# Kernel optimization log

Measured on AMD Instinct MI355X. Metric: run time of the kernel, lower is better.

The kernel has to match this reference:

```python
import jax, jax.numpy as jnp
import numpy as np


def _top_k_mask(matrix, k):
    # top-k along last dim, then scatter 1s into a zero mask (faithful to torch scatter_)
    D = matrix.shape[-1]
    flat = matrix.reshape(-1, D)                       # [N, D]
    _, idx = jax.lax.top_k(flat, k)                    # [N, k]
    rows = jnp.arange(flat.shape[0])[:, None]          # [N, 1]
    mask = jnp.zeros_like(flat).at[rows, idx].set(1.0)  # scatter ones
    return (flat * mask).reshape(matrix.shape)


def setup_inputs() -> dict:
    key = jax.random.key(0)
    x = jax.random.normal(key, (4, 4096, 4096), dtype=jnp.float32)
    return {"x": x, "k": 512}


def reference(x, k):
    g = jax.nn.gelu(x, approximate=False)  # torch F.gelu default is exact (erf) gelu
    return _top_k_mask(g, k)
```

## Files before the change

### kernel.cpp

```cpp
#include <hip/hip_runtime.h>

#define TG_D    4096
#define TG_BLK  256
#define TG_CAP  896
#define TG_T0   0.90f
#define TG_P16G 0xBF40u

__device__ __forceinline__ unsigned tg_key(float f) {
  unsigned b = __float_as_uint(f);
  return (b & 0x80000000u) ? ~b : (b | 0x80000000u);
}
__device__ __forceinline__ unsigned tg_dec(unsigned k) {
  return (k & 0x80000000u) ? (k & 0x7FFFFFFFu) : ~k;
}

__device__ __forceinline__ float tg_gelu(float x) {
#pragma clang fp contract(off)
  float d  = x / 0x1.6a09e6p+0f;
  float xc = fmaxf(fminf(d, 4.0f), -4.0f);
  float x2 = xc * xc;
  float p = -2.72614225801306e-10f;
  p = __builtin_fmaf(p, x2,  2.77068142495902e-08f);
  p = __builtin_fmaf(p, x2, -2.10102402082508e-06f);
  p = __builtin_fmaf(p, x2, -5.69250639462346e-05f);
  p = __builtin_fmaf(p, x2, -7.34990630326855e-04f);
  p = __builtin_fmaf(p, x2, -2.95459980854025e-03f);
  p = __builtin_fmaf(p, x2, -1.60960333262415e-02f);
  float q = -1.45660718464996e-05f;
  q = __builtin_fmaf(q, x2, -2.13374055278905e-04f);
  q = __builtin_fmaf(q, x2, -1.68282697438203e-03f);
  q = __builtin_fmaf(q, x2, -7.37332916720468e-03f);
  q = __builtin_fmaf(q, x2, -1.42647390514189e-02f);
  float num = xc * p;
  float e   = num / q;
  float s   = e + 1.0f;
  float m   = x * s;
  return m * 0.5f;
}

__device__ __forceinline__ void tg_pick_byte(unsigned (*h)[256], unsigned* wtot,
                                             unsigned* sel, unsigned kRem,
                                             int tid, int lane, int wv) {
  __syncthreads();
  unsigned cb = h[0][tid] + h[1][tid] + h[2][tid] + h[3][tid];
  unsigned v = cb;
#pragma unroll
  for (int d = 1; d < 64; d <<= 1) {
    unsigned o = __shfl_down(v, d, 64);
    v += (lane + d < 64) ? o : 0u;
  }
  if (lane == 0) wtot[wv] = v;
  __syncthreads();
  unsigned hi = 0;
#pragma unroll
  for (int w = 0; w < 4; ++w)
    if (w > wv) hi += wtot[w];
  unsigned sGE = v + hi, sGT = sGE - cb;
  if (sGE >= kRem && sGT < kRem) { sel[0] = (unsigned)tid; sel[1] = sGT; sel[2] = cb; }
  __syncthreads();
}

__global__ __launch_bounds__(TG_BLK) void topk_gelu_kernel(
    const float* __restrict__ x, const int* __restrict__ kptr,
    float* __restrict__ out) {
  __shared__ unsigned       ckey[TG_CAP];
  __shared__ unsigned short cidx[TG_CAP];
  __shared__ alignas(16) unsigned char uraw[TG_D * 4];
  __shared__ unsigned       skey[64];
  __shared__ unsigned short scidx[64];
  __shared__ unsigned short scpos[64];
  __shared__ unsigned       tieMask[128];
  __shared__ unsigned       wtot[4];
  __shared__ unsigned       sel[3];
  __shared__ unsigned       cnt2, mCnt;

  float*    cx  = (float*)uraw;
  unsigned (*hist)[256] = (unsigned (*)[256])(uraw + sizeof(float) * TG_CAP);
  float*    obuf = (float*)uraw;

  const int tid = threadIdx.x, lane = tid & 63, wv = tid >> 6;
  const unsigned k = (unsigned)(*kptr);
  const float* xr   = x   + (size_t)blockIdx.x * TG_D;
  float*       outr = out + (size_t)blockIdx.x * TG_D;

  hist[0][tid] = 0; hist[1][tid] = 0; hist[2][tid] = 0; hist[3][tid] = 0;
  if (tid == 0) { cnt2 = 0; mCnt = 0; sel[0] = 0; sel[1] = 0; sel[2] = 0; }

  float xv[16];
#pragma unroll
  for (int c = 0; c < 4; ++c) {
    float4 v = reinterpret_cast<const float4*>(xr)[tid + c * TG_BLK];
    xv[4*c+0] = v.x; xv[4*c+1] = v.y; xv[4*c+2] = v.z; xv[4*c+3] = v.w;
  }

  unsigned candMask = 0;
#pragma unroll
  for (int e = 0; e < 16; ++e)
    if (xv[e] >= TG_T0) candMask |= (1u << e);
  const unsigned cnt = (unsigned)__popc(candMask);
  unsigned inc = cnt;
#pragma unroll
  for (int d = 1; d < 64; d <<= 1) {
    unsigned o = __shfl_up(inc, d, 64);
    if (lane >= d) inc += o;
  }
  if (lane == 63) wtot[wv] = inc;
  __syncthreads();
  unsigned base = inc - cnt;
#pragma unroll
  for (int w = 0; w < 4; ++w) if (w < wv) base += wtot[w];
  const unsigned n0 = wtot[0] + wtot[1] + wtot[2] + wtot[3];
  const unsigned nC = n0 < (unsigned)TG_CAP ? n0 : (unsigned)TG_CAP;

  if (n0 <= (unsigned)TG_CAP) {
    unsigned p = base;
#pragma unroll
    for (int e = 0; e < 16; ++e)
      if (candMask & (1u << e)) {
        cx[p]   = xv[e];
        cidx[p] = (unsigned short)((tid + (e >> 2) * TG_BLK) * 4 + (e & 3));
        ++p;
      }
  }
  __syncthreads();

  unsigned myc2 = 0;
  for (unsigned i = tid; i < nC; i += TG_BLK) {
    unsigned kk = tg_key(tg_gelu(cx[i]));
    ckey[i] = kk;
    if (kk >= 0xC0000000u) ++myc2;
    else atomicAdd(&hist[wv][(kk >> 16) & 255], 1u);
  }
#pragma unroll
  for (int d = 1; d < 64; d <<= 1) {
    unsigned o = __shfl_down(myc2, d, 64);
    myc2 += (lane + d < 64) ? o : 0u;
  }
  if (lane == 0 && myc2) atomicAdd(&cnt2, myc2);
  __syncthreads();

  const unsigned c2v  = cnt2;
  const unsigned kRem = k - c2v;
  unsigned cb = hist[0][tid] + hist[1][tid] + hist[2][tid] + hist[3][tid];
  unsigned v = cb;
#pragma unroll
  for (int d = 1; d < 64; d <<= 1) {
    unsigned o = __shfl_down(v, d, 64);
    v += (lane + d < 64) ? o : 0u;
  }
  if (lane == 0) wtot[wv] = v;
  __syncthreads();
  unsigned hi = 0;
#pragma unroll
  for (int w = 0; w < 4; ++w) if (w > wv) hi += wtot[w];
  {
    unsigned sGE = v + hi, sGT = sGE - cb;
    if (sGE >= kRem && sGT < kRem) { sel[0] = (unsigned)tid; sel[1] = sGT; sel[2] = cb; }
  }
  __syncthreads();

  const unsigned p16   = 0xBF00u | sel[0];
  const unsigned kRem2 = kRem - sel[1];
  const unsigned m     = sel[2];
  const bool slow = (n0 > (unsigned)TG_CAP) || (c2v >= k) || (p16 < TG_P16G) ||
                    (m > 64u) || (kRem2 == 0u) || (kRem2 > m);

  if (slow) {
    unsigned gk[16];
#pragma unroll
    for (int e = 0; e < 16; ++e) gk[e] = tg_key(tg_gelu(xv[e]));
    unsigned prefix = 0, kRemS = k;
#pragma unroll
    for (int ps = 0; ps < 4; ++ps) {
      const int shift = 24 - 8 * ps;
      __syncthreads();
      hist[0][tid] = 0; hist[1][tid] = 0; hist[2][tid] = 0; hist[3][tid] = 0;
      __syncthreads();
      const unsigned pmask = ps ? (0xFFFFFFFFu << (shift + 8)) : 0u;
#pragma unroll
      for (int e = 0; e < 16; ++e)
        if ((gk[e] & pmask) == prefix) atomicAdd(&hist[wv][(gk[e] >> shift) & 255], 1u);
      tg_pick_byte(hist, wtot, sel, kRemS, tid, lane, wv);
      prefix |= sel[0] << shift;
      kRemS  -= sel[1];
    }
    const unsigned Tg = prefix, kRemF = kRemS, cntEq = sel[2];
    const bool needTie = (cntEq != kRemF);
    if (needTie) {
      if (tid < 128) tieMask[tid] = 0;
      __syncthreads();
#pragma unroll
      for (int e = 0; e < 16; ++e)
        if (gk[e] == Tg) {
          unsigned s = (unsigned)((tid + (e >> 2) * TG_BLK) * 4 + (e & 3));
          atomicOr(&tieMask[s >> 5], 1u << (s & 31));
        }
      __syncthreads();
    }
#pragma unroll
    for (int c = 0; c < 4; ++c) {
      float r[4];
#pragma unroll
      for (int j = 0; j < 4; ++j) {
        const int e = 4 * c + j;
        unsigned kk = gk[e];
        bool keep = kk > Tg;
        if (!keep && kk == Tg) {
          if (!needTie) keep = true;
          else {
            unsigned s = (unsigned)((tid + c * TG_BLK) * 4 + j);
            unsigned rank = __popc(tieMask[s >> 5] & ((1u << (s & 31)) - 1u));
            for (unsigned w = 0; w < (s >> 5); ++w) rank += __popc(tieMask[w]);
            keep = rank < kRemF;
          }
        }
        r[j] = keep ? __uint_as_float(tg_dec(kk)) : 0.0f;
      }
      float4 o4; o4.x = r[0]; o4.y = r[1]; o4.z = r[2]; o4.w = r[3];
      reinterpret_cast<float4*>(outr)[tid + c * TG_BLK] = o4;
    }
    return;
  }

  for (unsigned i = tid; i < n0; i += TG_BLK) {
    unsigned kk = ckey[i];
    if ((kk >> 16) == p16) {
      unsigned p = atomicAdd(&mCnt, 1u);
      if (p < 64u) { skey[p] = kk; scidx[p] = cidx[i]; scpos[p] = (unsigned short)i; }
    }
  }
  __syncthreads();

  if (wv == 0) {
    unsigned myk = (lane < (int)m) ? skey[lane] : 0u;
    unsigned myi = (lane < (int)m) ? (unsigned)scidx[lane] : 0xFFFFu;
    unsigned gt = 0, tr = 0;
    for (unsigned j = 0; j < m; ++j) {
      unsigned kj = __shfl(myk, (int)j, 64);
      unsigned ij = __shfl(myi, (int)j, 64);
      gt += (kj > myk) ? 1u : 0u;
      tr += (kj == myk && ij < myi) ? 1u : 0u;
    }
    if (lane < (int)m) ckey[scpos[lane]] = ((gt + tr) < kRem2) ? myk : 0u;
  }
  {
    float4 z4; z4.x = 0.f; z4.y = 0.f; z4.z = 0.f; z4.w = 0.f;
#pragma unroll
    for (int w = 0; w < 4; ++w)
      reinterpret_cast<float4*>(obuf)[tid + w * TG_BLK] = z4;
  }
  __syncthreads();

  for (unsigned i = tid; i < n0; i += TG_BLK) {
    unsigned kk = ckey[i];
    if ((kk >> 16) >= p16) obuf[cidx[i]] = __uint_as_float(tg_dec(kk));
  }
  __syncthreads();

#pragma unroll
  for (int c = 0; c < 4; ++c) {
    float4 o4 = reinterpret_cast<const float4*>(obuf)[tid + c * TG_BLK];
    reinterpret_cast<float4*>(outr)[tid + c * TG_BLK] = o4;
  }
}

extern "C" void kernel_launch(void* const* d_in, const int* in_sizes, int n_in,
                              void* d_out, int out_size, void* d_ws, size_t ws_size,
                              hipStream_t stream) {
  const float* x = (const float*)d_in[0];
  const int* kp  = (const int*)d_in[1];
  float* out     = (float*)d_out;
  int rows = in_sizes[0] / TG_D;
  topk_gelu_kernel<<<rows, TG_BLK, 0, stream>>>(x, kp, out);
}
```

Before: 101.2 us.

## Write fast-path output directly from registers with nontemporal stores, drop LDS staging buffer

Removes the LDS output staging buffer (zero-fill, scatter, read back) on the fast path. Each thread now rebuilds its own output from its candidate mask and the compacted keys, and writes it with nontemporal vector stores. Candidate keys are stored as raw float bits on the assumption that candidates are positive, which lets the threshold bins be retuned (T0 raised to 1.0, CAP lowered). A guard sends rows with too few candidates to the slow path, and the smaller shared memory footprint may allow more blocks per CU.

```diff
diff --git a/kernel.cpp b/kernel.cpp
--- a/kernel.cpp
+++ b/kernel.cpp
@@ -2,9 +2,11 @@
 
 #define TG_D    4096
 #define TG_BLK  256
-#define TG_CAP  896
-#define TG_T0   0.90f
-#define TG_P16G 0xBF40u
+#define TG_CAP  832
+#define TG_T0   1.00f
+#define TG_BING 0x3F58u
+
+typedef float v4f __attribute__((ext_vector_type(4)));
 
 __device__ __forceinline__ unsigned tg_key(float f) {
   unsigned b = __float_as_uint(f);
@@ -63,9 +65,10 @@
 __global__ __launch_bounds__(TG_BLK) void topk_gelu_kernel(
     const float* __restrict__ x, const int* __restrict__ kptr,
     float* __restrict__ out) {
+  __shared__ float          cx[TG_CAP];
   __shared__ unsigned       ckey[TG_CAP];
   __shared__ unsigned short cidx[TG_CAP];
-  __shared__ alignas(16) unsigned char uraw[TG_D * 4];
+  __shared__ unsigned       hist[4][256];
   __shared__ unsigned       skey[64];
   __shared__ unsigned short scidx[64];
   __shared__ unsigned short scpos[64];
@@ -74,10 +77,6 @@
   __shared__ unsigned       sel[3];
   __shared__ unsigned       cnt2, mCnt;
 
-  float*    cx  = (float*)uraw;
-  unsigned (*hist)[256] = (unsigned (*)[256])(uraw + sizeof(float) * TG_CAP);
-  float*    obuf = (float*)uraw;
-
   const int tid = threadIdx.x, lane = tid & 63, wv = tid >> 6;
   const unsigned k = (unsigned)(*kptr);
   const float* xr   = x   + (size_t)blockIdx.x * TG_D;
@@ -126,10 +125,10 @@
 
   unsigned myc2 = 0;
   for (unsigned i = tid; i < nC; i += TG_BLK) {
-    unsigned kk = tg_key(tg_gelu(cx[i]));
-    ckey[i] = kk;
-    if (kk >= 0xC0000000u) ++myc2;
-    else atomicAdd(&hist[wv][(kk >> 16) & 255], 1u);
+    unsigned gb = __float_as_uint(tg_gelu(cx[i]));
+    ckey[i] = gb;
+    if (gb >= 0x40000000u) ++myc2;
+    else atomicAdd(&hist[wv][(gb >> 16) & 255], 1u);
   }
 #pragma unroll
   for (int d = 1; d < 64; d <<= 1) {
@@ -159,11 +158,11 @@
   }
   __syncthreads();
 
-  const unsigned p16   = 0xBF00u | sel[0];
+  const unsigned bin   = 0x3F00u | sel[0];
   const unsigned kRem2 = kRem - sel[1];
   const unsigned m     = sel[2];
-  const bool slow = (n0 > (unsigned)TG_CAP) || (c2v >= k) || (p16 < TG_P16G) ||
-                    (m > 64u) || (kRem2 == 0u) || (kRem2 > m);
+  const bool slow = (n0 > (unsigned)TG_CAP) || (n0 < k + 32u) || (c2v >= k) ||
+                    (bin < TG_BING) || (m > 64u) || (kRem2 == 0u) || (kRem2 > m);
 
   if (slow) {
     unsigned gk[16];
@@ -216,17 +215,17 @@
         }
         r[j] = keep ? __uint_as_float(tg_dec(kk)) : 0.0f;
       }
-      float4 o4; o4.x = r[0]; o4.y = r[1]; o4.z = r[2]; o4.w = r[3];
-      reinterpret_cast<float4*>(outr)[tid + c * TG_BLK] = o4;
+      v4f o4 = { r[0], r[1], r[2], r[3] };
+      __builtin_nontemporal_store(o4, reinterpret_cast<v4f*>(outr) + tid + c * TG_BLK);
     }
     return;
   }
 
   for (unsigned i = tid; i < n0; i += TG_BLK) {
-    unsigned kk = ckey[i];
-    if ((kk >> 16) == p16) {
+    unsigned gb = ckey[i];
+    if ((gb >> 16) == bin) {
       unsigned p = atomicAdd(&mCnt, 1u);
-      if (p < 64u) { skey[p] = kk; scidx[p] = cidx[i]; scpos[p] = (unsigned short)i; }
+      if (p < 64u) { skey[p] = gb; scidx[p] = cidx[i]; scpos[p] = (unsigned short)i; }
     }
   }
   __syncthreads();
@@ -243,24 +242,25 @@
     }
     if (lane < (int)m) ckey[scpos[lane]] = ((gt + tr) < kRem2) ? myk : 0u;
   }
-  {
-    float4 z4; z4.x = 0.f; z4.y = 0.f; z4.z = 0.f; z4.w = 0.f;
-#pragma unroll
-    for (int w = 0; w < 4; ++w)
-      reinterpret_cast<float4*>(obuf)[tid + w * TG_BLK] = z4;
-  }
-  __syncthreads();
-
-  for (unsigned i = tid; i < n0; i += TG_BLK) {
-    unsigned kk = ckey[i];
-    if ((kk >> 16) >= p16) obuf[cidx[i]] = __uint_as_float(tg_dec(kk));
-  }
-  __syncthreads();
-
+  __syncthreads();
+
+  const unsigned thr = bin << 16;
+  unsigned p = base;
 #pragma unroll
   for (int c = 0; c < 4; ++c) {
-    float4 o4 = reinterpret_cast<const float4*>(obuf)[tid + c * TG_BLK];
-    reinterpret_cast<float4*>(outr)[tid + c * TG_BLK] = o4;
+    float r[4];
+#pragma unroll
+    for (int j = 0; j < 4; ++j) {
+      const int e = 4 * c + j;
+      float ov = 0.0f;
+      if (candMask & (1u << e)) {
+        unsigned gb = ckey[p++];
+        if (gb >= thr) ov = __uint_as_float(gb);
+      }
+      r[j] = ov;
+    }
+    v4f o4 = { r[0], r[1], r[2], r[3] };
+    __builtin_nontemporal_store(o4, reinterpret_cast<v4f*>(outr) + tid + c * TG_BLK);
   }
 }
 
```

Measured after the change: 85.41 us. 15.6% less time.
